# Kernel optimization log

Hardware: AMD Instinct MI355X
Metric: run time of the kernel (lower is better)

## Reference

```python
import jax, jax.numpy as jnp
import numpy as np

B, C, H, W = 8, 64, 64, 64
OUT_H, OUT_W = 32, 32


def setup_inputs() -> dict:
    key = jax.random.key(0)
    ks = jax.random.split(key, 9)
    s = 1.0 / np.sqrt(C).astype(np.float32)
    return {
        "x": jax.random.normal(ks[0], (B, C, H, W), jnp.float32),
        "wq": jax.random.normal(ks[1], (C, C), jnp.float32) * s,
        "bq": jax.random.normal(ks[2], (C,), jnp.float32) * 0.01,
        "wk": jax.random.normal(ks[3], (C, C), jnp.float32) * s,
        "bk": jax.random.normal(ks[4], (C,), jnp.float32) * 0.01,
        "wv": jax.random.normal(ks[5], (C, C), jnp.float32) * s,
        "bv": jax.random.normal(ks[6], (C,), jnp.float32) * 0.01,
        "wm": jax.random.normal(ks[7], (C, C), jnp.float32) * s,
        "bm": jax.random.normal(ks[8], (C,), jnp.float32) * 0.01,
    }


def reference(x, wq, bq, wk, bk, wv, bv, wm, bm):
    # pushforward: self-attention over spatial tokens, 1x1-conv mixing + ReLU,
    # then bilinear resize to out_shape (align_corners=False semantics).
    b, c, h, w = x.shape
    t = x.reshape(b, c, h * w).transpose(0, 2, 1)  # [B, HW, C] tokens
    q = jnp.einsum('bnc,dc->bnd', t, wq) + bq      # 1x1 conv == per-pixel linear
    k = jnp.einsum('bnc,dc->bnd', t, wk) + bk
    v = jnp.einsum('bnc,dc->bnd', t, wv) + bv
    scores = jnp.einsum('bnc,bmc->bnm', q, k) / jnp.sqrt(jnp.float32(c))  # [B, HW, HW]
    attn = jax.nn.softmax(scores, axis=-1)
    o = jnp.einsum('bnm,bmc->bnc', attn, v)        # [B, HW, C]
    mixed = jax.nn.relu(jnp.einsum('bnc,dc->bnd', o, wm) + bm)
    out = mixed.transpose(0, 2, 1).reshape(b, c, h, w)
    # F.interpolate(mode='bilinear', align_corners=False) == half-pixel bilinear, no antialias
    out = jax.image.resize(out, (b, c, OUT_H, OUT_W), method='bilinear', antialias=False)
    return out
```

## Files before the change

### kernel.cpp

```cpp
#include <hip/hip_runtime.h>
#include <stdint.h>

typedef unsigned short u16;
typedef unsigned int   u32;
typedef __attribute__((ext_vector_type(8)))  short short8;
typedef __attribute__((ext_vector_type(2)))  float f32x2;
typedef __attribute__((ext_vector_type(4)))  float f32x4;
typedef __attribute__((ext_vector_type(16))) float f32x16;

#define NTOK 4096
#define LOG2E 1.44269504088896340736f
#define QS    (0.125f * LOG2E)

__device__ __forceinline__ u16 f2bf(float f) {
    u32 u = __builtin_bit_cast(u32, f);
    u += 0x7fffu + ((u >> 16) & 1u);
    return (u16)(u >> 16);
}
__device__ __forceinline__ float bf2f(u16 v) {
    return __builtin_bit_cast(float, (u32)v << 16);
}
__device__ __forceinline__ u32 cvtpk(float a, float b) {
    u32 r;
    asm("v_cvt_pk_bf16_f32 %0, %1, %2" : "=v"(r) : "v"(a), "v"(b));
    return r;
}
__device__ __forceinline__ void pl32swap(u32 &a, u32 &b) {
    asm("v_permlane32_swap_b32 %0, %1" : "+v"(a), "+v"(b));
}
__device__ __forceinline__ f32x16 zero16() {
    f32x16 v;
#pragma unroll
    for (int i = 0; i < 16; ++i) v[i] = 0.f;
    return v;
}

#define MFMA16x32 __builtin_amdgcn_mfma_f32_16x16x32_bf16
#define MFMA32x16 __builtin_amdgcn_mfma_f32_32x32x16_bf16

__global__ __launch_bounds__(256) void qkv_mfma5(
    const float* __restrict__ x,
    const float* __restrict__ wq, const float* __restrict__ bq,
    const float* __restrict__ wk, const float* __restrict__ bk,
    const float* __restrict__ wv, const float* __restrict__ bv,
    u16* __restrict__ Q, u16* __restrict__ KF, u16* __restrict__ VF)
{
    __shared__ __align__(16) u16 Wl[3 * 64 * 72];
    __shared__ __align__(16) u16 Xl[64 * 64];
    const int tid  = threadIdx.x;
    const int b    = blockIdx.x & 7;
    const int slab = blockIdx.x >> 3;
    const int n0   = slab << 6;
    const int wave = tid >> 6;
    const int lane = tid & 63;
    const int quad = lane >> 4;
    const int l15  = lane & 15;

#pragma unroll
    for (int j = 0; j < 12; ++j) {
        const float* src = (j < 4) ? wq : (j < 8) ? wk : wv;
        const float sc = (j < 4) ? QS : 1.0f;
        const int idx = (j & 3) * 1024 + tid * 4;
        const float4 v = *(const float4*)(src + idx);
        uint2 pk;
        pk.x = (u32)f2bf(v.x * sc) | ((u32)f2bf(v.y * sc) << 16);
        pk.y = (u32)f2bf(v.z * sc) | ((u32)f2bf(v.w * sc) << 16);
        *(uint2*)&Wl[(j >> 2) * 4608 + (idx >> 6) * 72 + (idx & 63)] = pk;
    }

    float4 xs[4];
#pragma unroll
    for (int g = 0; g < 4; ++g) {
        const int ch = g * 16 + wave * 4 + quad;
        xs[g] = *(const float4*)(x + ((size_t)(b * 64 + ch)) * NTOK + n0 + l15 * 4);
    }
#pragma unroll
    for (int g = 0; g < 4; ++g) {
        const int ch = g * 16 + wave * 4 + quad;
        const float vv[4] = {xs[g].x, xs[g].y, xs[g].z, xs[g].w};
#pragma unroll
        for (int e = 0; e < 4; ++e) {
            const int tok = l15 * 4 + e;
            Xl[tok * 64 + (((ch >> 3) ^ (tok & 7)) & 7) * 8 + (ch & 7)] = f2bf(vv[e]);
        }
    }
    __syncthreads();

    const int row0 = wave * 16 + l15;
    short8 xf[2];
#pragma unroll
    for (int kk = 0; kk < 2; ++kk)
        xf[kk] = *(const short8*)&Xl[row0 * 64 + (((kk * 4 + quad) ^ (row0 & 7)) & 7) * 8];

    const size_t tokbase = (size_t)b * NTOK + n0 + wave * 16;

#pragma unroll
    for (int mat = 0; mat < 2; ++mat) {
        const float* bias = (mat == 0) ? bq : bk;
        const float bsc = (mat == 0) ? QS : 1.0f;
#pragma unroll
        for (int mt = 0; mt < 4; ++mt) {
            const u16* wr = &Wl[mat * 4608 + (mt * 16 + l15) * 72 + quad * 8];
            const short8 wf0 = *(const short8*)(wr);
            const short8 wf1 = *(const short8*)(wr + 32);
            f32x4 acc = {0.f, 0.f, 0.f, 0.f};
            acc = MFMA16x32(wf0, xf[0], acc, 0, 0, 0);
            acc = MFMA16x32(wf1, xf[1], acc, 0, 0, 0);
            const float4 b4 = *(const float4*)(bias + mt * 16 + quad * 4);
            uint2 pk;
            pk.x = (u32)f2bf(acc[0] + b4.x * bsc) | ((u32)f2bf(acc[1] + b4.y * bsc) << 16);
            pk.y = (u32)f2bf(acc[2] + b4.z * bsc) | ((u32)f2bf(acc[3] + b4.w * bsc) << 16);
            if (mat == 0) {
                *(uint2*)(Q + (tokbase + l15) * 64 + mt * 16 + quad * 4) = pk;
            } else {
                const int tokl = wave * 16 + l15;
                const int gt   = slab * 2 + (tokl >> 5);
                const int c31k = tokl & 31;
                const int hwk  = quad >> 1;
                const int j0   = (quad & 1) * 4;
                *(uint2*)(KF + (((size_t)b * 128 + gt) * 4 + mt) * 512
                             + (hwk * 32 + c31k) * 8 + j0) = pk;
            }
        }
    }

    __syncthreads();
    u16* Vl = Xl;
    const int tok = wave * 16 + l15;
#pragma unroll
    for (int mt = 0; mt < 4; ++mt) {
        const u16* wr = &Wl[2 * 4608 + (mt * 16 + l15) * 72 + quad * 8];
        const short8 wf0 = *(const short8*)(wr);
        const short8 wf1 = *(const short8*)(wr + 32);
        f32x4 acc = {0.f, 0.f, 0.f, 0.f};
        acc = MFMA16x32(wf0, xf[0], acc, 0, 0, 0);
        acc = MFMA16x32(wf1, xf[1], acc, 0, 0, 0);
        const float4 b4 = *(const float4*)(bv + mt * 16 + quad * 4);
        const float o[4] = {acc[0] + b4.x, acc[1] + b4.y, acc[2] + b4.z, acc[3] + b4.w};
#pragma unroll
        for (int r = 0; r < 4; ++r) {
            const int d = mt * 16 + quad * 4 + r;
            Vl[d * 64 + (((tok >> 3) ^ ((d >> 1) & 7)) & 7) * 8 + (tok & 7)] = f2bf(o[r]);
        }
    }
    __syncthreads();

#pragma unroll
    for (int dd = 0; dd < 4; ++dd) {
        const int d2   = (tid >> 4) + dd * 16;
        const int tok0 = (tid & 15) * 4;
        const int slot = ((tok0 >> 3) ^ ((d2 >> 1) & 7)) & 7;
        const uint2 v2 = *(const uint2*)&Vl[d2 * 64 + slot * 8 + (tok0 & 7)];
        const int gt  = slab * 2 + (tok0 >> 5);
        const int mk  = ((d2 >> 5) << 1) | ((tok0 & 31) >> 4);
        const int hwv = (tok0 >> 3) & 1;
        const int j   = tok0 & 7;
        *(uint2*)(VF + (((size_t)b * 128 + gt) * 4 + mk) * 512
                     + (hwv * 32 + (d2 & 31)) * 8 + j) = v2;
    }
}

__global__ __launch_bounds__(512, 2) void attn14(
    const u16* __restrict__ Q, const u16* __restrict__ KF,
    const u16* __restrict__ VF,
    const float* __restrict__ wm, const float* __restrict__ bm,
    float* __restrict__ out)
{
    __shared__ __align__(16) char smem[54272];
    const int tid  = threadIdx.x;
    const int wave = tid >> 6;
    const int lane = tid & 63;
    const int c31  = lane & 31;
    const int hw   = lane >> 5;
    const int quad = lane >> 4;
    const int l15  = lane & 15;
    const int h    = wave >> 2;
    const int s    = wave & 3;
    const int b    = blockIdx.x & 7;
    const int oh   = blockIdx.x >> 3;
    const int n0   = oh * 128;

    short8 qf[2][4];
#pragma unroll
    for (int nt = 0; nt < 2; ++nt)
#pragma unroll
        for (int ks = 0; ks < 4; ++ks)
            qf[nt][ks] = *(const short8*)(Q + ((size_t)(b * NTOK + n0 + h * 64 + nt * 32 + c31)) * 64
                                            + ks * 16 + hw * 8);

    const u16* KFb = KF + ((size_t)b * 128 + s * 32) * 2048;
    const u16* VFb = VF + ((size_t)b * 128 + s * 32) * 2048;
    const int l8 = lane * 8;

    f32x16 O[2][2];
#pragma unroll
    for (int mt = 0; mt < 2; ++mt)
#pragma unroll
        for (int nt = 0; nt < 2; ++nt) O[mt][nt] = zero16();
    float lpa[2] = {0.f, 0.f};

    auto load_k = [&](short8 (&kf)[4], int t) {
        const int tc = (t < 32) ? t : 31;
        const u16* kt = KFb + (size_t)tc * 2048;
#pragma unroll
        for (int ks = 0; ks < 4; ++ks)
            kf[ks] = *(const short8*)(kt + ks * 512 + l8);
    };
    auto load_v = [&](short8 (&vf)[4], int t) {
        const int tc = (t < 32) ? t : 31;
        const u16* vt = VFb + (size_t)tc * 2048;
#pragma unroll
        for (int mk = 0; mk < 4; ++mk)
            vf[mk] = *(const short8*)(vt + mk * 512 + l8);
    };

    auto stage = [&](short8 (&kf)[4], short8 (&vf)[4], int tnext) {
        f32x16 sv[2];
        __builtin_amdgcn_s_setprio(1);
#pragma unroll
        for (int nt = 0; nt < 2; ++nt) {
            f32x16 a = zero16();
            a = MFMA32x16(kf[0], qf[nt][0], a, 0, 0, 0);
            a = MFMA32x16(kf[1], qf[nt][1], a, 0, 0, 0);
            a = MFMA32x16(kf[2], qf[nt][2], a, 0, 0, 0);
            a = MFMA32x16(kf[3], qf[nt][3], a, 0, 0, 0);
            sv[nt] = a;
        }
        __builtin_amdgcn_s_setprio(0);
        load_k(kf, tnext);
        __builtin_amdgcn_sched_barrier(0);
#pragma unroll
        for (int nt = 0; nt < 2; ++nt) {
            float p[16];
#pragma unroll
            for (int r = 0; r < 16; ++r) p[r] = __builtin_amdgcn_exp2f(sv[nt][r]);
            const f32x2 a0 = {p[0],  p[1]},  a1 = {p[2],  p[3]};
            const f32x2 a2 = {p[4],  p[5]},  a3 = {p[6],  p[7]};
            const f32x2 a4 = {p[8],  p[9]},  a5 = {p[10], p[11]};
            const f32x2 a6 = {p[12], p[13]}, a7 = {p[14], p[15]};
            const f32x2 s0 = a0 + a1, s1 = a2 + a3, s2 = a4 + a5, s3 = a6 + a7;
            const f32x2 s4 = s0 + s1, s5 = s2 + s3;
            const f32x2 s6 = s4 + s5;
            lpa[nt] += s6.x + s6.y;
            u32 c0 = cvtpk(p[0],  p[1]),  c1 = cvtpk(p[2],  p[3]);
            u32 c2 = cvtpk(p[4],  p[5]),  c3 = cvtpk(p[6],  p[7]);
            u32 c4 = cvtpk(p[8],  p[9]),  c5 = cvtpk(p[10], p[11]);
            u32 c6 = cvtpk(p[12], p[13]), c7 = cvtpk(p[14], p[15]);
            pl32swap(c0, c2);  pl32swap(c1, c3);
            pl32swap(c4, c6);  pl32swap(c5, c7);
            uint4 B0, B1;
            B0.x = c0; B0.y = c1; B0.z = c2; B0.w = c3;
            B1.x = c4; B1.y = c5; B1.z = c6; B1.w = c7;
            const short8 pb0 = __builtin_bit_cast(short8, B0);
            const short8 pb1 = __builtin_bit_cast(short8, B1);
            __builtin_amdgcn_s_setprio(1);
            O[0][nt] = MFMA32x16(vf[0], pb0, O[0][nt], 0, 0, 0);
            O[0][nt] = MFMA32x16(vf[1], pb1, O[0][nt], 0, 0, 0);
            O[1][nt] = MFMA32x16(vf[2], pb0, O[1][nt], 0, 0, 0);
            O[1][nt] = MFMA32x16(vf[3], pb1, O[1][nt], 0, 0, 0);
            __builtin_amdgcn_s_setprio(0);
        }
        load_v(vf, tnext);
        __builtin_amdgcn_sched_barrier(0);
    };

    short8 kf0[4], vf0[4], kf1[4], vf1[4], kf2[4], vf2[4];
    load_k(kf0, 0); load_v(vf0, 0);
    load_k(kf1, 1); load_v(vf1, 1);
    load_k(kf2, 2); load_v(vf2, 2);

#pragma unroll 1
    for (int tt = 0; tt < 10; ++tt) {
        const int t0 = tt * 3;
        stage(kf0, vf0, t0 + 3);
        stage(kf1, vf1, t0 + 4);
        stage(kf2, vf2, t0 + 5);
    }
    stage(kf0, vf0, 31);
    stage(kf1, vf1, 31);

#pragma unroll
    for (int nt = 0; nt < 2; ++nt) lpa[nt] += __shfl_xor(lpa[nt], 32);

    float* lpbuf = (float*)(smem + 52224);
    if (hw == 0) {
#pragma unroll
        for (int nt = 0; nt < 2; ++nt)
            lpbuf[(h * 4 + s) * 64 + nt * 32 + c31] = lpa[nt];
    }
    if (s != 0) {
        u16* sec = (u16*)smem + (h * 3 + s - 1) * 4352;
#pragma unroll
        for (int mt = 0; mt < 2; ++mt)
#pragma unroll
            for (int nt = 0; nt < 2; ++nt)
#pragma unroll
                for (int r = 0; r < 16; ++r) {
                    const int ch = mt * 32 + (r & 3) + 8 * (r >> 2) + 4 * hw;
                    sec[(nt * 32 + c31) * 68 + ch] = f2bf(O[mt][nt][r]);
                }
    }
    __syncthreads();

    float rinv[2];
    if (s == 0) {
#pragma unroll
        for (int nt = 0; nt < 2; ++nt) {
            float sum = 0.f;
#pragma unroll
            for (int sx = 0; sx < 4; ++sx)
                sum += lpbuf[(h * 4 + sx) * 64 + nt * 32 + c31];
            rinv[nt] = 1.0f / sum;
        }
#pragma unroll
        for (int sx = 1; sx < 4; ++sx) {
            const u16* sec = (const u16*)smem + (h * 3 + sx - 1) * 4352;
#pragma unroll
            for (int mt = 0; mt < 2; ++mt)
#pragma unroll
                for (int nt = 0; nt < 2; ++nt)
#pragma unroll
                    for (int r = 0; r < 16; ++r) {
                        const int ch = mt * 32 + (r & 3) + 8 * (r >> 2) + 4 * hw;
                        O[mt][nt][r] += bf2f(sec[(nt * 32 + c31) * 68 + ch]);
                    }
        }
    }
    short8 wB[4][2];
    float bb[4];
#pragma unroll
    for (int nt = 0; nt < 4; ++nt) {
        const int d = nt * 16 + l15;
        const float* wr = wm + (size_t)d * 64 + quad * 8;
        const float4 a0 = *(const float4*)(wr);
        const float4 a1 = *(const float4*)(wr + 4);
        const float4 c0 = *(const float4*)(wr + 32);
        const float4 c1 = *(const float4*)(wr + 36);
        ((u32*)&wB[nt][0])[0] = (u32)f2bf(a0.x) | ((u32)f2bf(a0.y) << 16);
        ((u32*)&wB[nt][0])[1] = (u32)f2bf(a0.z) | ((u32)f2bf(a0.w) << 16);
        ((u32*)&wB[nt][0])[2] = (u32)f2bf(a1.x) | ((u32)f2bf(a1.y) << 16);
        ((u32*)&wB[nt][0])[3] = (u32)f2bf(a1.z) | ((u32)f2bf(a1.w) << 16);
        ((u32*)&wB[nt][1])[0] = (u32)f2bf(c0.x) | ((u32)f2bf(c0.y) << 16);
        ((u32*)&wB[nt][1])[1] = (u32)f2bf(c0.z) | ((u32)f2bf(c0.w) << 16);
        ((u32*)&wB[nt][1])[2] = (u32)f2bf(c1.x) | ((u32)f2bf(c1.y) << 16);
        ((u32*)&wB[nt][1])[3] = (u32)f2bf(c1.z) | ((u32)f2bf(c1.w) << 16);
        bb[nt] = bm[d];
    }
    __syncthreads();

    if (s == 0) {
        u16* M0 = (u16*)smem + h * 4096;
#pragma unroll
        for (int mt = 0; mt < 2; ++mt)
#pragma unroll
            for (int nt = 0; nt < 2; ++nt)
#pragma unroll
                for (int r = 0; r < 16; ++r) {
                    const int lr = nt * 32 + c31;
                    const int ch = mt * 32 + (r & 3) + 8 * (r >> 2) + 4 * hw;
                    const float v = O[mt][nt][r] * rinv[nt];
                    M0[lr * 64 + (((ch >> 3) ^ (lr & 7)) & 7) * 8 + (ch & 7)] = f2bf(v);
                }
    }
    __syncthreads();

    const u16* M0r = (const u16*)smem + (wave >> 2) * 4096;
    const int lr = (wave & 3) * 16 + l15;
    const short8 af0 = *(const short8*)&M0r[lr * 64 + ((quad ^ (lr & 7)) & 7) * 8];
    const short8 af1 = *(const short8*)&M0r[lr * 64 + (((4 + quad) ^ (lr & 7)) & 7) * 8];
    float* Mf = (float*)(smem + 16384);
#pragma unroll
    for (int nt = 0; nt < 4; ++nt) {
        f32x4 acc = {0.f, 0.f, 0.f, 0.f};
        acc = MFMA16x32(af0, wB[nt][0], acc, 0, 0, 0);
        acc = MFMA16x32(af1, wB[nt][1], acc, 0, 0, 0);
#pragma unroll
        for (int r = 0; r < 4; ++r) {
            float v = acc[r] + bb[nt];
            v = v > 0.f ? v : 0.f;
            Mf[(wave * 16 + quad * 4 + r) * 68 + nt * 16 + l15] = v;
        }
    }
    __syncthreads();

    const int ow = tid & 31;
    const int cb = (tid >> 5) & 15;
#pragma unroll
    for (int i = 0; i < 4; ++i) {
        const int c = cb + i * 16;
        const float v = 0.25f * (Mf[(2 * ow) * 68 + c] + Mf[(2 * ow + 1) * 68 + c]
                               + Mf[(64 + 2 * ow) * 68 + c] + Mf[(65 + 2 * ow) * 68 + c]);
        out[((size_t)(b * 64 + c) * 32 + oh) * 32 + ow] = v;
    }
}

extern "C" void kernel_launch(void* const* d_in, const int* in_sizes, int n_in,
                              void* d_out, int out_size, void* d_ws, size_t ws_size,
                              hipStream_t stream) {
    (void)in_sizes; (void)n_in; (void)out_size; (void)ws_size;
    const float* x  = (const float*)d_in[0];
    const float* wq = (const float*)d_in[1];
    const float* bq = (const float*)d_in[2];
    const float* wk = (const float*)d_in[3];
    const float* bk = (const float*)d_in[4];
    const float* wv = (const float*)d_in[5];
    const float* bv = (const float*)d_in[6];
    const float* wm = (const float*)d_in[7];
    const float* bm = (const float*)d_in[8];

    u16* Q  = (u16*)d_ws;
    u16* KF = Q + (size_t)8 * NTOK * 64;
    u16* VF = KF + (size_t)8 * NTOK * 64;

    qkv_mfma5<<<512, 256, 0, stream>>>(x, wq, bq, wk, bk, wv, bv, Q, KF, VF);
    attn14<<<256, 512, 0, stream>>>(Q, KF, VF, wm, bm, (float*)d_out);
}
```

Baseline: 121.4 us.

## Software-pipeline QK MFMA with softmax tail across tiles, double-buffer K/V

```diff
diff --git a/kernel.cpp b/kernel.cpp
--- a/kernel.cpp
+++ b/kernel.cpp
@@ -160,7 +160,7 @@
     }
 }
 
-__global__ __launch_bounds__(512, 2) void attn14(
+__global__ __launch_bounds__(512, 2) void attn16(
     const u16* __restrict__ Q, const u16* __restrict__ KF,
     const u16* __restrict__ VF,
     const float* __restrict__ wm, const float* __restrict__ bm,
@@ -214,70 +214,82 @@
             vf[mk] = *(const short8*)(vt + mk * 512 + l8);
     };
 
-    auto stage = [&](short8 (&kf)[4], short8 (&vf)[4], int tnext) {
-        f32x16 sv[2];
+    auto qk_nt = [&](f32x16 &sv, const short8 (&kf)[4], const short8 (&q)[4]) {
         __builtin_amdgcn_s_setprio(1);
-#pragma unroll
-        for (int nt = 0; nt < 2; ++nt) {
-            f32x16 a = zero16();
-            a = MFMA32x16(kf[0], qf[nt][0], a, 0, 0, 0);
-            a = MFMA32x16(kf[1], qf[nt][1], a, 0, 0, 0);
-            a = MFMA32x16(kf[2], qf[nt][2], a, 0, 0, 0);
-            a = MFMA32x16(kf[3], qf[nt][3], a, 0, 0, 0);
-            sv[nt] = a;
-        }
+        f32x16 a = zero16();
+        a = MFMA32x16(kf[0], q[0], a, 0, 0, 0);
+        a = MFMA32x16(kf[1], q[1], a, 0, 0, 0);
+        a = MFMA32x16(kf[2], q[2], a, 0, 0, 0);
+        a = MFMA32x16(kf[3], q[3], a, 0, 0, 0);
+        sv = a;
         __builtin_amdgcn_s_setprio(0);
-        load_k(kf, tnext);
+    };
+
+    auto tail_nt = [&](const f32x16 &sv, const short8 (&vf)[4],
+                       float &lp, f32x16 &O0, f32x16 &O1) {
+        float p[16];
+#pragma unroll
+        for (int r = 0; r < 16; ++r) p[r] = __builtin_amdgcn_exp2f(sv[r]);
+        const f32x2 a0 = {p[0],  p[1]},  a1 = {p[2],  p[3]};
+        const f32x2 a2 = {p[4],  p[5]},  a3 = {p[6],  p[7]};
+        const f32x2 a4 = {p[8],  p[9]},  a5 = {p[10], p[11]};
+        const f32x2 a6 = {p[12], p[13]}, a7 = {p[14], p[15]};
+        const f32x2 s0 = a0 + a1, s1 = a2 + a3, s2 = a4 + a5, s3 = a6 + a7;
+        const f32x2 s4 = s0 + s1, s5 = s2 + s3;
+        const f32x2 s6 = s4 + s5;
+        lp += s6.x + s6.y;
+        u32 c0 = cvtpk(p[0],  p[1]),  c1 = cvtpk(p[2],  p[3]);
+        u32 c2 = cvtpk(p[4],  p[5]),  c3 = cvtpk(p[6],  p[7]);
+        u32 c4 = cvtpk(p[8],  p[9]),  c5 = cvtpk(p[10], p[11]);
+        u32 c6 = cvtpk(p[12], p[13]), c7 = cvtpk(p[14], p[15]);
+        pl32swap(c0, c2);  pl32swap(c1, c3);
+        pl32swap(c4, c6);  pl32swap(c5, c7);
+        uint4 B0, B1;
+        B0.x = c0; B0.y = c1; B0.z = c2; B0.w = c3;
+        B1.x = c4; B1.y = c5; B1.z = c6; B1.w = c7;
+        const short8 pb0 = __builtin_bit_cast(short8, B0);
+        const short8 pb1 = __builtin_bit_cast(short8, B1);
+        __builtin_amdgcn_s_setprio(1);
+        O0 = MFMA32x16(vf[0], pb0, O0, 0, 0, 0);
+        O0 = MFMA32x16(vf[1], pb1, O0, 0, 0, 0);
+        O1 = MFMA32x16(vf[2], pb0, O1, 0, 0, 0);
+        O1 = MFMA32x16(vf[3], pb1, O1, 0, 0, 0);
+        __builtin_amdgcn_s_setprio(0);
+    };
+
+    short8 k0[4], v0[4], k1[4], v1[4];
+    load_k(k0, 0); load_v(v0, 0);
+    load_k(k1, 1); load_v(v1, 1);
+    f32x16 svA, svB;
+    qk_nt(svA, k0, qf[0]);
+
+#pragma unroll 1
+    for (int tt = 0; tt < 15; ++tt) {
+        const int t = tt * 2;
+        qk_nt(svB, k0, qf[1]);
+        load_k(k0, t + 2);
         __builtin_amdgcn_sched_barrier(0);
-#pragma unroll
-        for (int nt = 0; nt < 2; ++nt) {
-            float p[16];
-#pragma unroll
-            for (int r = 0; r < 16; ++r) p[r] = __builtin_amdgcn_exp2f(sv[nt][r]);
-            const f32x2 a0 = {p[0],  p[1]},  a1 = {p[2],  p[3]};
-            const f32x2 a2 = {p[4],  p[5]},  a3 = {p[6],  p[7]};
-            const f32x2 a4 = {p[8],  p[9]},  a5 = {p[10], p[11]};
-            const f32x2 a6 = {p[12], p[13]}, a7 = {p[14], p[15]};
-            const f32x2 s0 = a0 + a1, s1 = a2 + a3, s2 = a4 + a5, s3 = a6 + a7;
-            const f32x2 s4 = s0 + s1, s5 = s2 + s3;
-            const f32x2 s6 = s4 + s5;
-            lpa[nt] += s6.x + s6.y;
-            u32 c0 = cvtpk(p[0],  p[1]),  c1 = cvtpk(p[2],  p[3]);
-            u32 c2 = cvtpk(p[4],  p[5]),  c3 = cvtpk(p[6],  p[7]);
-            u32 c4 = cvtpk(p[8],  p[9]),  c5 = cvtpk(p[10], p[11]);
-            u32 c6 = cvtpk(p[12], p[13]), c7 = cvtpk(p[14], p[15]);
-            pl32swap(c0, c2);  pl32swap(c1, c3);
-            pl32swap(c4, c6);  pl32swap(c5, c7);
-            uint4 B0, B1;
-            B0.x = c0; B0.y = c1; B0.z = c2; B0.w = c3;
-            B1.x = c4; B1.y = c5; B1.z = c6; B1.w = c7;
-            const short8 pb0 = __builtin_bit_cast(short8, B0);
-            const short8 pb1 = __builtin_bit_cast(short8, B1);
-            __builtin_amdgcn_s_setprio(1);
-            O[0][nt] = MFMA32x16(vf[0], pb0, O[0][nt], 0, 0, 0);
-            O[0][nt] = MFMA32x16(vf[1], pb1, O[0][nt], 0, 0, 0);
-            O[1][nt] = MFMA32x16(vf[2], pb0, O[1][nt], 0, 0, 0);
-            O[1][nt] = MFMA32x16(vf[3], pb1, O[1][nt], 0, 0, 0);
-            __builtin_amdgcn_s_setprio(0);
-        }
-        load_v(vf, tnext);
+        tail_nt(svA, v0, lpa[0], O[0][0], O[1][0]);
+        qk_nt(svA, k1, qf[0]);
+        tail_nt(svB, v0, lpa[1], O[0][1], O[1][1]);
+        load_v(v0, t + 2);
         __builtin_amdgcn_sched_barrier(0);
-    };
-
-    short8 kf0[4], vf0[4], kf1[4], vf1[4], kf2[4], vf2[4];
-    load_k(kf0, 0); load_v(vf0, 0);
-    load_k(kf1, 1); load_v(vf1, 1);
-    load_k(kf2, 2); load_v(vf2, 2);
-
-#pragma unroll 1
-    for (int tt = 0; tt < 10; ++tt) {
-        const int t0 = tt * 3;
-        stage(kf0, vf0, t0 + 3);
-        stage(kf1, vf1, t0 + 4);
-        stage(kf2, vf2, t0 + 5);
-    }
-    stage(kf0, vf0, 31);
-    stage(kf1, vf1, 31);
+        qk_nt(svB, k1, qf[1]);
+        load_k(k1, t + 3);
+        __builtin_amdgcn_sched_barrier(0);
+        tail_nt(svA, v1, lpa[0], O[0][0], O[1][0]);
+        qk_nt(svA, k0, qf[0]);
+        tail_nt(svB, v1, lpa[1], O[0][1], O[1][1]);
+        load_v(v1, t + 3);
+        __builtin_amdgcn_sched_barrier(0);
+    }
+    qk_nt(svB, k0, qf[1]);
+    tail_nt(svA, v0, lpa[0], O[0][0], O[1][0]);
+    qk_nt(svA, k1, qf[0]);
+    tail_nt(svB, v0, lpa[1], O[0][1], O[1][1]);
+    qk_nt(svB, k1, qf[1]);
+    tail_nt(svA, v1, lpa[0], O[0][0], O[1][0]);
+    tail_nt(svB, v1, lpa[1], O[0][1], O[1][1]);
 
 #pragma unroll
     for (int nt = 0; nt < 2; ++nt) lpa[nt] += __shfl_xor(lpa[nt], 32);
@@ -413,5 +425,5 @@
     u16* VF = KF + (size_t)8 * NTOK * 64;
 
     qkv_mfma5<<<512, 256, 0, stream>>>(x, wq, bq, wk, bk, wv, bv, Q, KF, VF);
-    attn14<<<256, 512, 0, stream>>>(Q, KF, VF, wm, bm, (float*)d_out);
-}
+    attn16<<<256, 512, 0, stream>>>(Q, KF, VF, wm, bm, (float*)d_out);
+}
```

After: 124.7 us. 2.6% more time.
